# Kernel optimization log

Hardware: AMD Instinct MI355X
Metric: run time of the kernel (lower is better)

Reference implementation:

```python
import jax, jax.numpy as jnp
import numpy as np

THRESHOLD = 20.0
CIRCLE_OFFSETS = [(0, -3), (1, -3), (2, -2), (3, -1), (3, 0), (3, 1), (2, 2), (1, 3),
                  (0, 3), (-1, 3), (-2, 2), (-3, 1), (-3, 0), (-3, -1), (-2, -2), (-1, -3)]


def setup_inputs() -> dict:
    key = jax.random.key(0)
    image = jax.random.uniform(key, (4, 1, 1080, 1920), dtype=jnp.float32) * 255.0
    return {"image": image}


def _detect_9_consecutive(bits_16):
    # bits_16: int32 (N, H, W). Build 24-bit circular buffer, test all 16 rotations
    # for 9 consecutive set bits (window == 511) using arithmetic-only ops.
    lower_8 = bits_16 % 256
    buffer_24 = bits_16 + lower_8 * 65536  # (N, H, W) int32
    divisors = (jnp.int32(2) ** jnp.arange(16, dtype=jnp.int32)).reshape(16, 1, 1, 1)
    shifted = (buffer_24[None] // divisors) % 512  # (16, N, H, W)
    return jnp.any(shifted == 511, axis=0)  # (N, H, W) bool


def reference(image):
    N, C, H, W = image.shape
    img = image.astype(jnp.float32)
    # Replicate-pad by 3 and gather the 16 Bresenham circle pixels via shifted slices.
    padded = jnp.pad(img[:, 0], ((0, 0), (3, 3), (3, 3)), mode='edge')  # (N, H+6, W+6)
    circle = jnp.stack(
        [padded[:, 3 + dy:3 + dy + H, 3 + dx:3 + dx + W] for dy, dx in CIRCLE_OFFSETS],
        axis=-1)  # (N, H, W, 16)
    center = img[:, 0][..., None]  # (N, H, W, 1)
    diff = circle - center
    powers = (jnp.int32(1) << jnp.arange(16, dtype=jnp.int32)).reshape(1, 1, 1, 16)
    dark_bits = ((diff >= THRESHOLD).astype(jnp.int32) * powers).sum(axis=-1)
    bright_bits = ((diff <= -THRESHOLD).astype(jnp.int32) * powers).sum(axis=-1)
    detected = _detect_9_consecutive(dark_bits) | _detect_9_consecutive(bright_bits)
    return detected.astype(jnp.float32)[:, None]  # (N, 1, H, W)
```

## Files before the change

### kernel.cpp

```cpp
#include <hip/hip_runtime.h>

#define IMG_H 1080
#define IMG_W 1920
#define TILE_W 64
#define TILE_H 4
#define SW 70
#define SH 10
#define SP 72

__device__ __forceinline__ unsigned det9(unsigned m) {
    unsigned x = m | (m << 16);
    unsigned t = x & (x >> 1);
    t &= t >> 2;
    t &= t >> 4;
    t &= x >> 8;
    return t;
}

#define STEP_GE(m, sc, val, thr)                                          \
    asm("v_cmp_ge_f32 %1, %2, %3\n\tv_addc_co_u32 %0, %1, %0, %0, %1"     \
        : "+v"(m), "=s"(sc) : "v"(val), "v"(thr))
#define STEP_LE(m, sc, val, thr)                                          \
    asm("v_cmp_le_f32 %1, %2, %3\n\tv_addc_co_u32 %0, %1, %0, %0, %1"     \
        : "+v"(m), "=s"(sc) : "v"(val), "v"(thr))

__global__ __launch_bounds__(256) void fast_score_kernel(const float* __restrict__ img,
                                                         float* __restrict__ out) {
    __shared__ float sm[SH * SP];

    const int n  = blockIdx.z;
    const int x0 = blockIdx.x * TILE_W;
    const int y0 = blockIdx.y * TILE_H;
    const int tid = threadIdx.x;

    const float* in = img + (size_t)n * (IMG_H * IMG_W);
    float* op = out + (size_t)n * (IMG_H * IMG_W);

    for (int i = tid; i < SH * SW; i += 256) {
        const int r = i / SW;
        const int c = i - r * SW;
        int gy = min(max(y0 - 3 + r, 0), IMG_H - 1);
        int gx = min(max(x0 - 3 + c, 0), IMG_W - 1);
        sm[r * SP + c] = in[(size_t)gy * IMG_W + gx];
    }
    __syncthreads();

    const int tx = tid & 63;
    const int ty = tid >> 6;
    const float* base = &sm[(ty + 3) * SP + (tx + 3)];

    constexpr int DY[16] = {0, 1, 2, 3, 3, 3, 2, 1, 0, -1, -2, -3, -3, -3, -2, -1};
    constexpr int DX[16] = {-3, -3, -2, -1, 0, 1, 2, 3, 3, 3, 2, 1, 0, -1, -2, -3};

    const float center = base[0];
    float t[16];
#pragma unroll
    for (int k = 0; k < 16; ++k) {
        t[k] = base[DY[k] * SP + DX[k]];
    }

    const float hi = center + 20.0f;
    const float lo = center - 20.0f;
    unsigned dark = 0u, bright = 0u;
    unsigned long long sc0, sc1;
#pragma unroll
    for (int k = 0; k < 16; ++k) {
        STEP_GE(dark,   sc0, t[k], hi);
        STEP_LE(bright, sc1, t[k], lo);
    }

    const float res = (det9(dark) | det9(bright)) ? 1.0f : 0.0f;
    op[(size_t)(y0 + ty) * IMG_W + (x0 + tx)] = res;
}

extern "C" void kernel_launch(void* const* d_in, const int* in_sizes, int n_in,
                              void* d_out, int out_size, void* d_ws, size_t ws_size,
                              hipStream_t stream) {
    const float* img = (const float*)d_in[0];
    float* out = (float*)d_out;
    const int n_img = in_sizes[0] / (IMG_H * IMG_W);
    dim3 grid(IMG_W / TILE_W,
              IMG_H / TILE_H,
              n_img);
    fast_score_kernel<<<grid, 256, 0, stream>>>(img, out);
}
```

Measured before the change: 108.5 us.

## Replace shared-memory tiling with direct global loads per row

Drops the LDS tile and __syncthreads, so each thread loads its 17 stencil values straight from global memory with clamped row and column indices. Each block now covers one row of 256 pixels, and reuse across neighbouring pixels is left to the L1/L2 caches. This removes the barrier and the LDS staging overhead. In exchange it issues many more global load instructions and relies on the caches to absorb the redundant reads. The last column block runs partially idle, since 1920 is not a multiple of 256.

Measured after the change: 99.27 us. 1.09x faster.

```diff
diff --git a/kernel.cpp b/kernel.cpp
--- a/kernel.cpp
+++ b/kernel.cpp
@@ -2,11 +2,6 @@
 
 #define IMG_H 1080
 #define IMG_W 1920
-#define TILE_W 64
-#define TILE_H 4
-#define SW 70
-#define SH 10
-#define SP 72
 
 __device__ __forceinline__ unsigned det9(unsigned m) {
     unsigned x = m | (m << 16);
@@ -26,37 +21,33 @@
 
 __global__ __launch_bounds__(256) void fast_score_kernel(const float* __restrict__ img,
                                                          float* __restrict__ out) {
-    __shared__ float sm[SH * SP];
+    const int n  = blockIdx.z;
+    const int y  = blockIdx.y;
+    const int gx = blockIdx.x * 256 + threadIdx.x;
 
-    const int n  = blockIdx.z;
-    const int x0 = blockIdx.x * TILE_W;
-    const int y0 = blockIdx.y * TILE_H;
-    const int tid = threadIdx.x;
+    const float* base = img + (size_t)n * (IMG_H * IMG_W);
 
-    const float* in = img + (size_t)n * (IMG_H * IMG_W);
-    float* op = out + (size_t)n * (IMG_H * IMG_W);
+    const float* rp[7];
+#pragma unroll
+    for (int d = 0; d < 7; ++d) {
+        const int ry = min(max(y + d - 3, 0), IMG_H - 1);
+        rp[d] = base + (size_t)ry * IMG_W;
+    }
 
-    for (int i = tid; i < SH * SW; i += 256) {
-        const int r = i / SW;
-        const int c = i - r * SW;
-        int gy = min(max(y0 - 3 + r, 0), IMG_H - 1);
-        int gx = min(max(x0 - 3 + c, 0), IMG_W - 1);
-        sm[r * SP + c] = in[(size_t)gy * IMG_W + gx];
+    int c[7];
+#pragma unroll
+    for (int d = 0; d < 7; ++d) {
+        c[d] = min(max(gx + d - 3, 0), IMG_W - 1);
     }
-    __syncthreads();
-
-    const int tx = tid & 63;
-    const int ty = tid >> 6;
-    const float* base = &sm[(ty + 3) * SP + (tx + 3)];
 
     constexpr int DY[16] = {0, 1, 2, 3, 3, 3, 2, 1, 0, -1, -2, -3, -3, -3, -2, -1};
     constexpr int DX[16] = {-3, -3, -2, -1, 0, 1, 2, 3, 3, 3, 2, 1, 0, -1, -2, -3};
 
-    const float center = base[0];
+    const float center = rp[3][c[3]];
     float t[16];
 #pragma unroll
     for (int k = 0; k < 16; ++k) {
-        t[k] = base[DY[k] * SP + DX[k]];
+        t[k] = rp[DY[k] + 3][c[DX[k] + 3]];
     }
 
     const float hi = center + 20.0f;
@@ -70,7 +61,9 @@
     }
 
     const float res = (det9(dark) | det9(bright)) ? 1.0f : 0.0f;
-    op[(size_t)(y0 + ty) * IMG_W + (x0 + tx)] = res;
+    if (gx < IMG_W) {
+        out[(size_t)n * (IMG_H * IMG_W) + (size_t)y * IMG_W + gx] = res;
+    }
 }
 
 extern "C" void kernel_launch(void* const* d_in, const int* in_sizes, int n_in,
@@ -79,8 +72,8 @@
     const float* img = (const float*)d_in[0];
     float* out = (float*)d_out;
     const int n_img = in_sizes[0] / (IMG_H * IMG_W);
-    dim3 grid(IMG_W / TILE_W,
-              IMG_H / TILE_H,
+    dim3 grid((IMG_W + 255) / 256,
+              IMG_H,
               n_img);
     fast_score_kernel<<<grid, 256, 0, stream>>>(img, out);
 }
```
